# Kernel tuning notes

Measured on AMD Instinct MI355X. Metric: run time of the kernel, lower is better.

## Reference

```python
import jax, jax.numpy as jnp
import numpy as np

WS = 8          # window size
NUM_HEADS = 12


def setup_inputs() -> dict:
    key = jax.random.key(0)
    k1, k2, k3 = jax.random.split(key, 3)
    B, N, C = 16, 4096, 384
    x = jax.random.normal(k1, (B, N, C), dtype=jnp.float32)
    # torch Linear weights stored as [in, out] so forward is x @ W
    qkv_w = jax.random.normal(k2, (C, 3 * C), dtype=jnp.float32) * (C ** -0.5)
    proj_w = jax.random.normal(k3, (C, C), dtype=jnp.float32) * (C ** -0.5)
    proj_b = jnp.zeros((C,), dtype=jnp.float32)
    return {"x": x, "qkv_w": qkv_w, "proj_w": proj_w, "proj_b": proj_b}


def reference(x, qkv_w, proj_w, proj_b):
    B, N, C = x.shape
    H = W = int(np.sqrt(N))
    hg, wg = H // WS, W // WS
    G = hg * wg
    nh = NUM_HEADS
    hd = C // nh
    scale = hd ** -0.5

    # window partition: [B, N, C] -> [B, hg, wg, ws, ws, C]
    xw = x.reshape(B, hg, WS, wg, WS, C).transpose(0, 1, 3, 2, 4, 5)
    xw = xw.reshape(B, G, WS * WS, C)

    # qkv projection -> [3, B, G, nh, ws*ws, hd]
    qkv = (xw @ qkv_w).reshape(B, G, WS * WS, 3, nh, hd)
    qkv = qkv.transpose(3, 0, 1, 4, 2, 5)
    q, k, v = qkv[0], qkv[1], qkv[2]

    attn = jnp.einsum('bgnqd,bgnkd->bgnqk', q, k) * scale
    attn = jax.nn.softmax(attn, axis=-1)
    out = jnp.einsum('bgnqk,bgnkd->bgnqd', attn, v)

    # merge heads and reverse window partition
    out = out.transpose(0, 1, 3, 2, 4).reshape(B, hg, wg, WS, WS, C)
    out = out.transpose(0, 1, 3, 2, 4, 5).reshape(B, N, C)

    return out @ proj_w + proj_b
```

## Files before the change

kernel.cpp:

```cpp
#include <hip/hip_runtime.h>
#include <stdint.h>

typedef unsigned short ushort_t;
typedef __bf16 bf16x8 __attribute__((ext_vector_type(8)));
typedef float floatx4 __attribute__((ext_vector_type(4)));
typedef float floatx16 __attribute__((ext_vector_type(16)));
typedef unsigned short ushort8 __attribute__((ext_vector_type(8)));

__device__ __forceinline__ ushort_t f2b(float f) {
  union { float f; unsigned u; } v; v.f = f;
  unsigned r = v.u + 0x7fffu + ((v.u >> 16) & 1u);
  return (ushort_t)(r >> 16);
}
__device__ __forceinline__ ushort_t b2u(float f) {
  union { __bf16 b; ushort_t u; } v; v.b = (__bf16)f; return v.u;
}
__device__ __forceinline__ bf16x8 cvt8(const float* p) {
  floatx4 f0 = *(const floatx4*)p;
  floatx4 f1 = *(const floatx4*)(p + 4);
  union { bf16x8 v; __bf16 e[8]; } u;
#pragma unroll
  for (int j = 0; j < 4; ++j) u.e[j] = (__bf16)f0[j];
#pragma unroll
  for (int j = 0; j < 4; ++j) u.e[4 + j] = (__bf16)f1[j];
  return u.v;
}

__device__ __forceinline__ unsigned cvtpk(float a, float b) {
  unsigned r;
  asm("v_cvt_pk_bf16_f32 %0, %1, %2" : "=v"(r) : "v"(a), "v"(b));
  return r;
}
__device__ __forceinline__ void plswap(unsigned& x, unsigned& y) {
  asm("v_permlane32_swap_b32 %0, %1" : "+v"(x), "+v"(y));
}

__device__ __forceinline__ void async16(const ushort_t* g, ushort_t* l) {
  __builtin_amdgcn_global_load_lds(
      (const __attribute__((address_space(1))) void*)g,
      (__attribute__((address_space(3))) void*)l, 16, 0, 0);
}

__global__ void transpose_k(const float* __restrict__ src,
                            ushort_t* __restrict__ dst, int R, int Cc) {
  int idx = blockIdx.x * 256 + threadIdx.x;
  if (idx < R * Cc) {
    int r = idx / Cc, c = idx % Cc;
    dst[(size_t)c * R + r] = f2b(src[idx]);
  }
}

__global__ __launch_bounds__(256) void gemm_qkv(
    const float* __restrict__ A,
    const ushort_t* __restrict__ Bt,
    ushort_t* __restrict__ C, int M, int N, int K) {
  __shared__ __align__(16) ushort_t As[128 * 64];
  __shared__ __align__(16) ushort_t Bs[128 * 64];
  const int t = threadIdx.x;
  const int nwg = gridDim.x;
  const int per = nwg >> 3;
  const int swz = (blockIdx.x & 7) * per + (blockIdx.x >> 3);
  const int ntn = N >> 7;
  const int m0 = (swz / ntn) << 7;
  const int n0 = (swz % ntn) << 7;
  const int w = t >> 6, lane = t & 63;
  const int wy = (w >> 1) << 6;
  const int wx = (w & 1) << 6;
  const int l15 = lane & 15;
  const int quad = lane >> 4;
  const int quad4 = quad << 2;
  floatx4 acc[4][4] = {};
  const int srow = t >> 3;
  const int sc = (((t & 7) ^ (srow & 7)) << 3);
  const float* gA = A + (size_t)(m0 + srow) * K + sc;
  const ushort_t* gB = Bt + (size_t)(n0 + srow) * K + sc;
  for (int k0 = 0; k0 < K; k0 += 64) {
    __syncthreads();
#pragma unroll
    for (int r4 = 0; r4 < 4; ++r4) {
      async16(gB + (size_t)r4 * 32 * K + k0, &Bs[r4 * 2048 + t * 8]);
      bf16x8 av = cvt8(gA + (size_t)r4 * 32 * K + k0);
      *(bf16x8*)&As[r4 * 2048 + t * 8] = av;
    }
    __syncthreads();
#pragma unroll
    for (int kk = 0; kk < 2; ++kk) {
      bf16x8 af[4], bfr[4];
#pragma unroll
      for (int i = 0; i < 4; ++i) {
        int row = wy + i * 16 + l15;
        af[i] = *(const bf16x8*)&As[row * 64 + ((((kk << 2) | quad) ^ (row & 7)) << 3)];
      }
#pragma unroll
      for (int j = 0; j < 4; ++j) {
        int row = wx + j * 16 + l15;
        bfr[j] = *(const bf16x8*)&Bs[row * 64 + ((((kk << 2) | quad) ^ (row & 7)) << 3)];
      }
#pragma unroll
      for (int i = 0; i < 4; ++i)
#pragma unroll
        for (int j = 0; j < 4; ++j)
          acc[i][j] = __builtin_amdgcn_mfma_f32_16x16x32_bf16(
              af[i], bfr[j], acc[i][j], 0, 0, 0);
    }
  }
#pragma unroll
  for (int i = 0; i < 4; ++i) {
#pragma unroll
    for (int r = 0; r < 4; ++r) {
      size_t row = (size_t)(m0 + wy + i * 16 + quad4 + r);
      ushort_t* cp = C + row * N + (n0 + wx + l15);
#pragma unroll
      for (int j = 0; j < 4; ++j) cp[j * 16] = f2b(acc[i][j][r]);
    }
  }
}

__global__ __launch_bounds__(256, 3) void attn_proj(
    const ushort_t* __restrict__ QKV, const ushort_t* __restrict__ Bt,
    const float* __restrict__ bias, float* __restrict__ out) {
  __shared__ __align__(16) ushort_t Ao[64 * 384];
  const int blk = blockIdx.x;
  const int b = blk >> 6, g = blk & 63;
  const int gy = g >> 3, gx = g & 7;
  const int t = threadIdx.x, w = t >> 6, lane = t & 63;
  const int l31 = lane & 31, bh = lane >> 5;
  const int l15 = lane & 15, quad = lane >> 4, quad4 = quad << 2;
  const size_t bbase = (size_t)b * 4096 + (size_t)(gy * 8) * 64 + gx * 8;
  const float scale = 0.17677669529663687f;

  for (int hi = 0; hi < 3; ++hi) {
    const int h = w * 3 + hi;
    const size_t hq = (size_t)h * 32;

    bf16x8 qf[2][2];
#pragma unroll
    for (int qt = 0; qt < 2; ++qt) {
      int tok = qt * 32 + l31;
      size_t row = bbase + (size_t)(tok >> 3) * 64 + (tok & 7);
#pragma unroll
      for (int dc = 0; dc < 2; ++dc)
        qf[qt][dc] = *(const bf16x8*)(QKV + row * 1152 + hq + dc * 16 + bh * 8);
    }
    bf16x8 kf[2][2];
#pragma unroll
    for (int kt = 0; kt < 2; ++kt) {
      int tok = kt * 32 + l31;
      size_t row = bbase + (size_t)(tok >> 3) * 64 + (tok & 7);
#pragma unroll
      for (int dc = 0; dc < 2; ++dc)
        kf[kt][dc] = *(const bf16x8*)(QKV + row * 1152 + 384 + hq + dc * 16 + bh * 8);
    }
    bf16x8 vf[4];
#pragma unroll
    for (int s = 0; s < 4; ++s) {
      const ushort_t* vbase =
          QKV + (bbase + (size_t)(2 * s + bh) * 64) * 1152 + 768 + hq + l31;
      union { ushort_t e[8]; bf16x8 v; } vu;
#pragma unroll
      for (int j = 0; j < 8; ++j) vu.e[j] = vbase[(size_t)j * 1152];
      vf[s] = vu.v;
    }

    floatx16 st[2][2] = {};
#pragma unroll
    for (int kt = 0; kt < 2; ++kt)
#pragma unroll
      for (int qt = 0; qt < 2; ++qt)
#pragma unroll
        for (int dc = 0; dc < 2; ++dc)
          st[kt][qt] = __builtin_amdgcn_mfma_f32_32x32x16_bf16(
              kf[kt][dc], qf[qt][dc], st[kt][qt], 0, 0, 0);

    float rs[2] = {0.f, 0.f};
#pragma unroll
    for (int kt = 0; kt < 2; ++kt)
#pragma unroll
      for (int qt = 0; qt < 2; ++qt)
#pragma unroll
        for (int r = 0; r < 16; ++r) {
          float e = __expf(st[kt][qt][r] * scale);
          st[kt][qt][r] = e;
          rs[qt] += e;
        }
#pragma unroll
    for (int qt = 0; qt < 2; ++qt) rs[qt] += __shfl_xor(rs[qt], 32);
    float inv[2] = {1.0f / rs[0], 1.0f / rs[1]};

    floatx16 o[2] = {};
#pragma unroll
    for (int s = 0; s < 4; ++s) {
      const int kt = s >> 1, r1x = (s & 1) << 1;
#pragma unroll
      for (int qt = 0; qt < 2; ++qt) {
        float iv = inv[qt];
        unsigned x0 = cvtpk(st[kt][qt][4 * r1x + 0] * iv, st[kt][qt][4 * r1x + 1] * iv);
        unsigned x1 = cvtpk(st[kt][qt][4 * r1x + 2] * iv, st[kt][qt][4 * r1x + 3] * iv);
        unsigned y0 = cvtpk(st[kt][qt][4 * r1x + 4] * iv, st[kt][qt][4 * r1x + 5] * iv);
        unsigned y1 = cvtpk(st[kt][qt][4 * r1x + 6] * iv, st[kt][qt][4 * r1x + 7] * iv);
        plswap(x0, y0);
        plswap(x1, y1);
        union { unsigned d[4]; bf16x8 v; } pa;
        pa.d[0] = x0; pa.d[1] = x1; pa.d[2] = y0; pa.d[3] = y1;
        o[qt] = __builtin_amdgcn_mfma_f32_32x32x16_bf16(pa.v, vf[s], o[qt], 0, 0, 0);
      }
    }

    const int base64 = (h >> 1) << 6;
    const int cbase = ((h & 1) << 2) | (l31 >> 3);
    const int e7 = l31 & 7;
#pragma unroll
    for (int qt = 0; qt < 2; ++qt)
#pragma unroll
      for (int r = 0; r < 16; ++r) {
        int tok = qt * 32 + (r & 3) + 8 * (r >> 2) + 4 * bh;
        int c = cbase ^ (tok & 7);
        Ao[tok * 384 + base64 + (c << 3) + e7] = b2u(o[qt][r]);
      }
  }

  __syncthreads();

  floatx4 acc[4][6] = {};
  for (int ks = 0; ks < 12; ++ks) {
    bf16x8 af[4];
#pragma unroll
    for (int i = 0; i < 4; ++i) {
      int row = i * 16 + l15;
      int c = (((ks & 1) << 2) | quad) ^ (row & 7);
      af[i] = *(const bf16x8*)&Ao[row * 384 + ((ks >> 1) << 6) + (c << 3)];
    }
    bf16x8 bfr[6];
#pragma unroll
    for (int j = 0; j < 6; ++j) {
      int n = w * 96 + j * 16 + l15;
      bfr[j] = *(const bf16x8*)&Bt[(size_t)n * 384 + ks * 32 + (quad << 3)];
    }
#pragma unroll
    for (int i = 0; i < 4; ++i)
#pragma unroll
      for (int j = 0; j < 6; ++j)
        acc[i][j] = __builtin_amdgcn_mfma_f32_16x16x32_bf16(
            af[i], bfr[j], acc[i][j], 0, 0, 0);
  }

  float bv[6];
#pragma unroll
  for (int j = 0; j < 6; ++j) bv[j] = bias[w * 96 + j * 16 + l15];
#pragma unroll
  for (int i = 0; i < 4; ++i) {
#pragma unroll
    for (int r = 0; r < 4; ++r) {
      int tok = i * 16 + quad4 + r;
      size_t grow = bbase + (size_t)(tok >> 3) * 64 + (tok & 7);
      float* cp = out + grow * 384 + w * 96 + l15;
#pragma unroll
      for (int j = 0; j < 6; ++j) cp[j * 16] = acc[i][j][r] + bv[j];
    }
  }
}

extern "C" void kernel_launch(void* const* d_in, const int* in_sizes, int n_in,
                              void* d_out, int out_size, void* d_ws, size_t ws_size,
                              hipStream_t stream) {
  const float* x      = (const float*)d_in[0];
  const float* qkv_w  = (const float*)d_in[1];
  const float* proj_w = (const float*)d_in[2];
  const float* proj_b = (const float*)d_in[3];
  float* out = (float*)d_out;

  const int M = 16 * 4096;
  const size_t need =
      ((size_t)M * 1152 + 1152 * 384 + 384 * 384) * 2;
  if (ws_size < need) return;

  ushort_t* qkv    = (ushort_t*)d_ws;
  ushort_t* qkvwT  = qkv + (size_t)M * 1152;
  ushort_t* projwT = qkvwT + (size_t)1152 * 384;

  transpose_k<<<(384 * 1152 + 255) / 256, 256, 0, stream>>>(qkv_w, qkvwT, 384, 1152);
  transpose_k<<<(384 * 384 + 255) / 256, 256, 0, stream>>>(proj_w, projwT, 384, 384);

  gemm_qkv<<<(M / 128) * (1152 / 128), 256, 0, stream>>>(
      x, qkvwT, qkv, M, 1152, 384);

  attn_proj<<<16 * 64, 256, 0, stream>>>(qkv, projwT, proj_b, out);
}
```

Baseline: 367.8 us.

## Pre-convert x to bf16 and load both GEMM operands async into LDS

Adds a separate kernel that converts x from fp32 to bf16 once. The QKV GEMM can then stream both A and B tiles through global_load_lds instead of loading fp32 and converting in registers. The MFMA operand order is also swapped so each lane holds four consecutive output columns, which allows packed 8-byte bf16 stores instead of scalar 2-byte stores. The cost is an extra full pass over x: reading it as fp32 and writing a bf16 copy. The GEMM then re-reads that copy 9 times, but at half the bytes, and its main loop loses the conversion ALU work.

```diff
diff --git a/kernel.cpp b/kernel.cpp
--- a/kernel.cpp
+++ b/kernel.cpp
@@ -39,6 +39,12 @@
   __builtin_amdgcn_global_load_lds(
       (const __attribute__((address_space(1))) void*)g,
       (__attribute__((address_space(3))) void*)l, 16, 0, 0);
+}
+
+__global__ __launch_bounds__(256) void cvt_x(const float* __restrict__ src,
+                                             ushort_t* __restrict__ dst, int n8) {
+  int i = blockIdx.x * 256 + threadIdx.x;
+  if (i < n8) *(bf16x8*)&dst[(size_t)i * 8] = cvt8(src + (size_t)i * 8);
 }
 
 __global__ void transpose_k(const float* __restrict__ src,
@@ -50,8 +56,8 @@
   }
 }
 
-__global__ __launch_bounds__(256) void gemm_qkv(
-    const float* __restrict__ A,
+__global__ __launch_bounds__(256) void gemm_bt(
+    const ushort_t* __restrict__ A,
     const ushort_t* __restrict__ Bt,
     ushort_t* __restrict__ C, int M, int N, int K) {
   __shared__ __align__(16) ushort_t As[128 * 64];
@@ -72,15 +78,14 @@
   floatx4 acc[4][4] = {};
   const int srow = t >> 3;
   const int sc = (((t & 7) ^ (srow & 7)) << 3);
-  const float* gA = A + (size_t)(m0 + srow) * K + sc;
+  const ushort_t* gA = A + (size_t)(m0 + srow) * K + sc;
   const ushort_t* gB = Bt + (size_t)(n0 + srow) * K + sc;
   for (int k0 = 0; k0 < K; k0 += 64) {
     __syncthreads();
 #pragma unroll
     for (int r4 = 0; r4 < 4; ++r4) {
+      async16(gA + (size_t)r4 * 32 * K + k0, &As[r4 * 2048 + t * 8]);
       async16(gB + (size_t)r4 * 32 * K + k0, &Bs[r4 * 2048 + t * 8]);
-      bf16x8 av = cvt8(gA + (size_t)r4 * 32 * K + k0);
-      *(bf16x8*)&As[r4 * 2048 + t * 8] = av;
     }
     __syncthreads();
 #pragma unroll
@@ -97,21 +102,22 @@
         bfr[j] = *(const bf16x8*)&Bs[row * 64 + ((((kk << 2) | quad) ^ (row & 7)) << 3)];
       }
 #pragma unroll
-      for (int i = 0; i < 4; ++i)
-#pragma unroll
-        for (int j = 0; j < 4; ++j)
-          acc[i][j] = __builtin_amdgcn_mfma_f32_16x16x32_bf16(
-              af[i], bfr[j], acc[i][j], 0, 0, 0);
-    }
-  }
-#pragma unroll
-  for (int i = 0; i < 4; ++i) {
-#pragma unroll
-    for (int r = 0; r < 4; ++r) {
-      size_t row = (size_t)(m0 + wy + i * 16 + quad4 + r);
-      ushort_t* cp = C + row * N + (n0 + wx + l15);
-#pragma unroll
-      for (int j = 0; j < 4; ++j) cp[j * 16] = f2b(acc[i][j][r]);
+      for (int jj = 0; jj < 4; ++jj)
+#pragma unroll
+        for (int ii = 0; ii < 4; ++ii)
+          acc[jj][ii] = __builtin_amdgcn_mfma_f32_16x16x32_bf16(
+              bfr[jj], af[ii], acc[jj][ii], 0, 0, 0);
+    }
+  }
+#pragma unroll
+  for (int ii = 0; ii < 4; ++ii) {
+    size_t row = (size_t)(m0 + wy + ii * 16 + l15);
+#pragma unroll
+    for (int jj = 0; jj < 4; ++jj) {
+      union { __bf16 e[4]; uint64_t v; } u;
+#pragma unroll
+      for (int r = 0; r < 4; ++r) u.e[r] = (__bf16)acc[jj][ii][r];
+      *(uint64_t*)&C[row * N + (n0 + wx + jj * 16 + quad4)] = u.v;
     }
   }
 }
@@ -271,18 +277,20 @@
 
   const int M = 16 * 4096;
   const size_t need =
-      ((size_t)M * 1152 + 1152 * 384 + 384 * 384) * 2;
+      ((size_t)M * 1152 + (size_t)M * 384 + 1152 * 384 + 384 * 384) * 2;
   if (ws_size < need) return;
 
   ushort_t* qkv    = (ushort_t*)d_ws;
-  ushort_t* qkvwT  = qkv + (size_t)M * 1152;
+  ushort_t* xb     = qkv + (size_t)M * 1152;
+  ushort_t* qkvwT  = xb + (size_t)M * 384;
   ushort_t* projwT = qkvwT + (size_t)1152 * 384;
 
+  cvt_x<<<(M * 384 / 8 + 255) / 256, 256, 0, stream>>>(x, xb, M * 384 / 8);
   transpose_k<<<(384 * 1152 + 255) / 256, 256, 0, stream>>>(qkv_w, qkvwT, 384, 1152);
   transpose_k<<<(384 * 384 + 255) / 256, 256, 0, stream>>>(proj_w, projwT, 384, 384);
 
-  gemm_qkv<<<(M / 128) * (1152 / 128), 256, 0, stream>>>(
-      x, qkvwT, qkv, M, 1152, 384);
+  gemm_bt<<<(M / 128) * (1152 / 128), 256, 0, stream>>>(
+      xb, qkvwT, qkv, M, 1152, 384);
 
   attn_proj<<<16 * 64, 256, 0, stream>>>(qkv, projwT, proj_b, out);
 }
```

Result: faster. 357.5 us (-2.8%).
